# Kernel tuning notes

Measured on AMD Instinct MI355X. Metric: run time of the kernel, lower is better.

Reference implementation:

```python
import jax, jax.numpy as jnp
import numpy as np
import math

B, S, E, H = 4, 2048, 1024, 1024  # batch, seq, n_embd, head_size


def _rope(q, k, pos):
    # q, k: (B, S, H); pos: (B, S) float
    d = q.shape[-1]
    omega = 1.0 / (10000.0 ** (jnp.arange(d // 2, dtype=jnp.float32) / (d / 2.0)))
    ang = pos[..., None] * omega                      # (B, S, d/2)
    sin = jnp.sin(ang)
    cos = jnp.cos(ang)
    cos_pos = jnp.repeat(cos, 2, axis=-1)             # (B, S, d) [c0,c0,c1,c1,...]
    sin_pos = jnp.repeat(sin, 2, axis=-1)

    def rot(t):
        t_ = jnp.stack([-t[..., 1::2], t[..., 0::2]], axis=-1).reshape(t.shape)
        return t * cos_pos + t_ * sin_pos

    return rot(q), rot(k)


def setup_inputs() -> dict:
    key = jax.random.key(0)
    ks = jax.random.split(key, 9)
    s = 1.0 / math.sqrt(E)
    x = jax.random.normal(ks[0], (B, S, E), dtype=jnp.float32)
    pos = jnp.broadcast_to(jnp.arange(S, dtype=jnp.float32), (B, S))
    mask = jnp.triu(jnp.ones((S, S), dtype=bool), k=1)  # causal: True = masked out
    Wq = jax.random.normal(ks[1], (H, E), dtype=jnp.float32) * s
    Wk = jax.random.normal(ks[2], (H, E), dtype=jnp.float32) * s
    Wv = jax.random.normal(ks[3], (H, E), dtype=jnp.float32) * s
    bq = jax.random.normal(ks[4], (H,), dtype=jnp.float32) * 0.01
    bk = jax.random.normal(ks[5], (H,), dtype=jnp.float32) * 0.01
    bv = jax.random.normal(ks[6], (H,), dtype=jnp.float32) * 0.01
    Wo = jax.random.normal(ks[7], (H, H), dtype=jnp.float32) * (1.0 / math.sqrt(H))
    bo = jax.random.normal(ks[8], (H,), dtype=jnp.float32) * 0.01
    return {"x": x, "pos": pos, "mask": mask, "Wq": Wq, "bq": bq,
            "Wk": Wk, "bk": bk, "Wv": Wv, "bv": bv, "Wo": Wo, "bo": bo}


def reference(x, pos, mask, Wq, bq, Wk, bk, Wv, bv, Wo, bo):
    n_embd = x.shape[-1]
    q = jnp.einsum('bse,he->bsh', x, Wq) + bq
    k = jnp.einsum('bse,he->bsh', x, Wk) + bk
    v = jnp.einsum('bse,he->bsh', x, Wv) + bv
    q, k = _rope(q, k, pos)
    # NOTE: original divides by sqrt(x.shape[-1]) == sqrt(n_embd), not sqrt(head_size)
    w = jnp.einsum('bqh,bkh->bqk', q, k) / jnp.sqrt(jnp.float32(n_embd))
    w = jnp.where(mask, jnp.float32(-1e7), w)
    w = jax.nn.softmax(w, axis=-1)  # dropout is identity in eval mode
    out = jnp.einsum('bqk,bkh->bqh', w, v)
    out = jnp.einsum('bsh,oh->bso', out, Wo) + bo
    return out
```

## Files before the change

kernel.cpp:

```cpp
#include <hip/hip_runtime.h>
#include <hip/hip_bf16.h>
#include <stdint.h>

typedef __attribute__((ext_vector_type(4))) float  f32x4;
typedef __attribute__((ext_vector_type(8))) short  short8;
typedef __attribute__((ext_vector_type(8))) __bf16 bf16x8;

#define GLB_AS __attribute__((address_space(1)))
#define LDS_AS __attribute__((address_space(3)))

__device__ __forceinline__ float bf2f(ushort u) {
    union { uint u32; float f; } c; c.u32 = (uint)u << 16; return c.f;
}
__device__ __forceinline__ ushort f2bf(float f) {
    union { float f; uint u32; } c; c.f = f;
    uint x = c.u32;
    return (ushort)((x + 0x7fffu + ((x >> 16) & 1u)) >> 16);
}

__device__ __forceinline__ void storeC(float* p, float v)  { *p = v; }
__device__ __forceinline__ void storeC(ushort* p, float v) { *p = f2bf(v); }

template<int N> __device__ __forceinline__ void vmwait() {
    if constexpr (N == 0) asm volatile("s_waitcnt vmcnt(0)" ::: "memory");
    else if constexpr (N == 6) asm volatile("s_waitcnt vmcnt(6)" ::: "memory");
}

__global__ __launch_bounds__(256) void convert_f32_bf16(
    const float* __restrict__ in, ushort* __restrict__ out, long n)
{
    long i0 = ((long)blockIdx.x * 256 + threadIdx.x) * 8;
    long stride = (long)gridDim.x * 256 * 8;
    for (long i = i0; i < n; i += stride) {
        float4 a = *(const float4*)(in + i);
        float4 b = *(const float4*)(in + i + 4);
        short8 o;
        o[0] = (short)f2bf(a.x); o[1] = (short)f2bf(a.y);
        o[2] = (short)f2bf(a.z); o[3] = (short)f2bf(a.w);
        o[4] = (short)f2bf(b.x); o[5] = (short)f2bf(b.y);
        o[6] = (short)f2bf(b.z); o[7] = (short)f2bf(b.w);
        *(short8*)(out + i) = o;
    }
}

__global__ __launch_bounds__(256) void rope_inplace(
    ushort* __restrict__ qk, const float* __restrict__ pos)
{
    const int row = blockIdx.x;
    const float p = pos[row];
    const size_t base = (size_t)row * 2048;
    const int tid = threadIdx.x;
#pragma unroll
    for (int t = 0; t < 2; ++t) {
        int j = tid + t * 256;
        float omega = exp2f(-(float)j * (13.287712379549449f / 512.0f));
        float ang = p * omega;
        float sn, cs;
        sincosf(ang, &sn, &cs);
        uint pq = *(uint*)(qk + base + 2 * j);
        float q0 = bf2f((ushort)(pq & 0xffff)), q1 = bf2f((ushort)(pq >> 16));
        float r0 = q0 * cs - q1 * sn, r1 = q1 * cs + q0 * sn;
        *(uint*)(qk + base + 2 * j) = (uint)f2bf(r0) | ((uint)f2bf(r1) << 16);
        uint pk = *(uint*)(qk + base + 1024 + 2 * j);
        float k0 = bf2f((ushort)(pk & 0xffff)), k1 = bf2f((ushort)(pk >> 16));
        float s0 = k0 * cs - k1 * sn, s1 = k1 * cs + k0 * sn;
        *(uint*)(qk + base + 1024 + 2 * j) = (uint)f2bf(s0) | ((uint)f2bf(s1) << 16);
    }
}

__global__ __launch_bounds__(256) void softmax_rows(ushort* __restrict__ P)
{
    const size_t base = (size_t)blockIdx.x * 2048;
    const int tid = threadIdx.x;
    const int lane = tid & 63, wid = tid >> 6;
    short8 v = *(const short8*)(P + base + tid * 8);
    float f[8];
#pragma unroll
    for (int j = 0; j < 8; ++j) f[j] = bf2f((ushort)v[j]);
    float mx = f[0];
#pragma unroll
    for (int j = 1; j < 8; ++j) mx = fmaxf(mx, f[j]);
#pragma unroll
    for (int o = 32; o; o >>= 1) mx = fmaxf(mx, __shfl_xor(mx, o, 64));
    __shared__ float redm[4], reds[4];
    if (lane == 0) redm[wid] = mx;
    __syncthreads();
    mx = fmaxf(fmaxf(redm[0], redm[1]), fmaxf(redm[2], redm[3]));
    float s = 0.f;
#pragma unroll
    for (int j = 0; j < 8; ++j) { f[j] = __expf(f[j] - mx); s += f[j]; }
#pragma unroll
    for (int o = 32; o; o >>= 1) s += __shfl_xor(s, o, 64);
    if (lane == 0) reds[wid] = s;
    __syncthreads();
    s = reds[0] + reds[1] + reds[2] + reds[3];
    float inv = 1.0f / s;
    short8 o8;
#pragma unroll
    for (int j = 0; j < 8; ++j) o8[j] = (short)f2bf(f[j] * inv);
    *(short8*)(P + base + tid * 8) = o8;
}


template<int BUF, int HALF>
__device__ __forceinline__ void stageT(ushort (&L)[2][2][8192],
    const ushort* __restrict__ G, int tileBase, int ld, int tk,
    int wid, int sr, int scS)
{
#pragma unroll
    for (int i = 0; i < 2; ++i) {
        const int chunk = wid * 2 + i;
        const ushort* g = G + (size_t)(tileBase + HALF * 128 + chunk * 8 + sr) * ld
                        + tk * 64 + scS * 8;
        __builtin_amdgcn_global_load_lds((const GLB_AS void*)g,
            (LDS_AS void*)(&L[BUF][HALF][chunk * 512]), 16, 0, 0);
    }
}

template<int BUF, int HALF>
__device__ __forceinline__ void readA(const ushort (&As)[2][2][8192],
    short8 (&afr)[4][2], int wr, int fr, int kg)
{
    const int sw = (fr & 7) << 3;
#pragma unroll
    for (int m = 0; m < 4; ++m) {
        const int r = wr * 64 + m * 16 + fr;
#pragma unroll
        for (int kk = 0; kk < 2; ++kk)
            afr[m][kk] = *(const short8*)&As[BUF][HALF][r * 64 + ((kk * 32 + kg * 8) ^ sw)];
    }
}

template<int BUF, int HALF>
__device__ __forceinline__ void readB(const ushort (&Bs)[2][2][8192],
    short8 (&bfr)[2][2], int wc, int fr, int kg)
{
    const int sw = (fr & 7) << 3;
#pragma unroll
    for (int n = 0; n < 2; ++n) {
        const int r = wc * 32 + n * 16 + fr;
#pragma unroll
        for (int kk = 0; kk < 2; ++kk)
            bfr[n][kk] = *(const short8*)&Bs[BUF][HALF][r * 64 + ((kk * 32 + kg * 8) ^ sw)];
    }
}

template<int MQ, int NQ>
__device__ __forceinline__ void domfma(f32x4 (&acc)[2][2][4][2],
    const short8 (&afr)[4][2], const short8 (&bfr)[2][2])
{
#pragma unroll
    for (int kk = 0; kk < 2; ++kk)
#pragma unroll
        for (int m = 0; m < 4; ++m)
#pragma unroll
            for (int n = 0; n < 2; ++n)
                acc[MQ][NQ][m][n] = __builtin_amdgcn_mfma_f32_16x16x32_bf16(
                    __builtin_bit_cast(bf16x8, afr[m][kk]),
                    __builtin_bit_cast(bf16x8, bfr[n][kk]),
                    acc[MQ][NQ][m][n], 0, 0, 0);
}

#define PHASE_MID() \
    __builtin_amdgcn_s_barrier(); \
    asm volatile("s_waitcnt lgkmcnt(0)" ::: "memory"); \
    __builtin_amdgcn_sched_barrier(0); \
    __builtin_amdgcn_s_setprio(1)
#define PHASE_END() \
    __builtin_amdgcn_s_setprio(0); \
    __builtin_amdgcn_s_barrier()

template<int BUF, int MODE>
__device__ __forceinline__ void group(
    ushort (&As)[2][2][8192], ushort (&Bs)[2][2][8192],
    f32x4 (&acc)[2][2][4][2],
    const ushort* __restrict__ A, const ushort* __restrict__ B,
    int rowBase, int colBase, int lda, int ldb, int t,
    int wid, int wr, int wc, int fr, int kg, int sr, int scS)
{
    short8 afr[4][2], bfr[2][2];
    readA<BUF, 0>(As, afr, wr, fr, kg);
    readB<BUF, 0>(Bs, bfr, wc, fr, kg);
    if constexpr (MODE != 2) stageT<BUF ^ 1, 0>(As, A, rowBase, lda, t + 1, wid, sr, scS);
    asm volatile("s_waitcnt lgkmcnt(8)" ::: "memory");
    PHASE_MID();
    domfma<0, 0>(acc, afr, bfr);
    PHASE_END();
    readA<BUF, 1>(As, afr, wr, fr, kg);
    if constexpr (MODE == 0) stageT<BUF, 0>(Bs, B, colBase, ldb, t + 2, wid, sr, scS);
    PHASE_MID();
    domfma<1, 0>(acc, afr, bfr);
    PHASE_END();
    readB<BUF, 1>(Bs, bfr, wc, fr, kg);
    if constexpr (MODE == 0) stageT<BUF, 1>(As, A, rowBase, lda, t + 2, wid, sr, scS);
    PHASE_MID();
    domfma<1, 1>(acc, afr, bfr);
    PHASE_END();
    readA<BUF, 0>(As, afr, wr, fr, kg);
    if constexpr (MODE == 0) stageT<BUF, 1>(Bs, B, colBase, ldb, t + 2, wid, sr, scS);
    PHASE_MID();
    domfma<0, 1>(acc, afr, bfr);
    __builtin_amdgcn_s_setprio(0);
    if constexpr (MODE == 0) vmwait<6>();
    else if constexpr (MODE == 1) vmwait<0>();
    __builtin_amdgcn_s_barrier();
}

template<bool BIAS_COL, bool BIAS_ROW, bool CAUSAL_MASK, bool CAUSAL_K, typename OutT>
__global__ __launch_bounds__(512, 2) void gemm256(
    const ushort* __restrict__ A, const ushort* __restrict__ B,
    OutT* __restrict__ C, const float* __restrict__ bias,
    int K, int lda, int ldb, int ldc,
    long sA, long sB, long sC, float scale)
{
    __shared__ ushort As[2][2][8192];
    __shared__ ushort Bs[2][2][8192];

    const int nx = gridDim.x, ny = gridDim.y;
    int flat = blockIdx.x + nx * (blockIdx.y + ny * blockIdx.z);
    const int nwg = nx * ny * gridDim.z;
    const int qq = nwg >> 3;
    int swz = (flat & 7) * qq + (flat >> 3);
    const int bx = swz % nx;
    int rest = swz / nx;
    const int by = rest % ny;
    const int bz = rest / ny;

    A += (long)bz * sA;
    B += (long)bz * sB;
    C += (long)bz * sC;
    const int tid = threadIdx.x;
    const int lane = tid & 63;
    const int wid = tid >> 6;
    const int wr = wid >> 2, wc = wid & 3;
    const int rowBase = by * 256;
    const int colBase = bx * 256;
    const int fr = lane & 15;
    const int kg = lane >> 4;

    f32x4 acc[2][2][4][2] = {};

    const bool skip = CAUSAL_MASK && (colBase > rowBase + 255);
    int Kend = K;
    if (CAUSAL_K) { int ke = rowBase + 256; Kend = ke < K ? ke : K; }

    if (!skip) {
        const int sr = lane >> 3;
        const int scS = (lane & 7) ^ (lane >> 3);
        stageT<0, 0>(As, A, rowBase, lda, 0, wid, sr, scS);
        stageT<0, 0>(Bs, B, colBase, ldb, 0, wid, sr, scS);
        stageT<0, 1>(As, A, rowBase, lda, 0, wid, sr, scS);
        stageT<0, 1>(Bs, B, colBase, ldb, 0, wid, sr, scS);
        stageT<1, 0>(Bs, B, colBase, ldb, 1, wid, sr, scS);
        stageT<1, 1>(As, A, rowBase, lda, 1, wid, sr, scS);
        stageT<1, 1>(Bs, B, colBase, ldb, 1, wid, sr, scS);
        vmwait<6>();
        __builtin_amdgcn_s_barrier();

        const int NT = Kend >> 6;
        int t = 0;
        for (; t + 3 < NT; t += 2) {
            group<0, 0>(As, Bs, acc, A, B, rowBase, colBase, lda, ldb, t,
                        wid, wr, wc, fr, kg, sr, scS);
            group<1, 0>(As, Bs, acc, A, B, rowBase, colBase, lda, ldb, t + 1,
                        wid, wr, wc, fr, kg, sr, scS);
        }
        group<0, 1>(As, Bs, acc, A, B, rowBase, colBase, lda, ldb, t,
                    wid, wr, wc, fr, kg, sr, scS);
        group<1, 2>(As, Bs, acc, A, B, rowBase, colBase, lda, ldb, t + 1,
                    wid, wr, wc, fr, kg, sr, scS);
    }

#pragma unroll
    for (int mq = 0; mq < 2; ++mq)
#pragma unroll
        for (int nq = 0; nq < 2; ++nq)
#pragma unroll
            for (int m = 0; m < 4; ++m)
#pragma unroll
                for (int n = 0; n < 2; ++n)
#pragma unroll
                    for (int j = 0; j < 4; ++j) {
                        int row = rowBase + mq * 128 + wr * 64 + m * 16 + kg * 4 + j;
                        int col = colBase + nq * 128 + wc * 32 + n * 16 + fr;
                        float v = acc[mq][nq][m][n][j] * scale;
                        if (BIAS_COL) v += bias[col];
                        if (BIAS_ROW) v += bias[row];
                        if (CAUSAL_MASK && (col > row)) v = -1e7f;
                        storeC(C + (size_t)row * ldc + col, v);
                    }
}

extern "C" void kernel_launch(void* const* d_in, const int* in_sizes, int n_in,
                              void* d_out, int out_size, void* d_ws, size_t ws_size,
                              hipStream_t stream)
{
    const float* x   = (const float*)d_in[0];
    const float* pos = (const float*)d_in[1];
    const float* Wq = (const float*)d_in[3]; const float* bq = (const float*)d_in[4];
    const float* Wk = (const float*)d_in[5]; const float* bk = (const float*)d_in[6];
    const float* Wv = (const float*)d_in[7]; const float* bv = (const float*)d_in[8];
    const float* Wo = (const float*)d_in[9]; const float* bo = (const float*)d_in[10];
    float* out = (float*)d_out;

    const int S = 2048, E = 1024, H = 1024, Bz = 4;
    const int Mtot = Bz * S;

    ushort* xb   = (ushort*)d_ws;
    ushort* wqkb = xb   + (size_t)Mtot * E;
    ushort* wvb  = wqkb + (size_t)2 * H * E;
    ushort* wob  = wvb  + (size_t)H * E;
    ushort* qk   = wob  + (size_t)H * H;
    ushort* vt   = qk   + (size_t)Mtot * 2 * H;
    ushort* P    = vt   + (size_t)H * Mtot;
    float*  bqk  = (float*)(P + (size_t)Bz * S * S);
    ushort* O    = xb;

    convert_f32_bf16<<<2048, 256, 0, stream>>>(x,  xb,   (long)Mtot * E);
    convert_f32_bf16<<<512,  256, 0, stream>>>(Wq, wqkb, (long)H * E);
    convert_f32_bf16<<<512,  256, 0, stream>>>(Wk, wqkb + (size_t)H * E, (long)H * E);
    convert_f32_bf16<<<512,  256, 0, stream>>>(Wv, wvb,  (long)H * E);
    convert_f32_bf16<<<512,  256, 0, stream>>>(Wo, wob,  (long)H * H);
    hipMemcpyAsync(bqk,     bq, H * sizeof(float), hipMemcpyDeviceToDevice, stream);
    hipMemcpyAsync(bqk + H, bk, H * sizeof(float), hipMemcpyDeviceToDevice, stream);

    gemm256<true, false, false, false, ushort><<<dim3(8, 32, 1), 512, 0, stream>>>(
        xb, wqkb, qk, bqk, E, E, E, 2 * H, 0, 0, 0, 1.0f);
    gemm256<false, true, false, false, ushort><<<dim3(32, 4, 1), 512, 0, stream>>>(
        wvb, xb, vt, bv, E, E, E, Mtot, 0, 0, 0, 1.0f);

    rope_inplace<<<Mtot, 256, 0, stream>>>(qk, pos);

    gemm256<false, false, true, false, ushort><<<dim3(8, 8, Bz), 512, 0, stream>>>(
        qk, qk + H, P, nullptr, H, 2 * H, 2 * H, S,
        (long)S * 2 * H, (long)S * 2 * H, (long)S * S, 0.03125f);

    softmax_rows<<<Mtot, 256, 0, stream>>>(P);

    gemm256<false, false, false, true, ushort><<<dim3(4, 8, Bz), 512, 0, stream>>>(
        P, vt, O, nullptr, S, S, Mtot, H,
        (long)S * S, (long)S, (long)S * H, 1.0f);

    gemm256<true, false, false, false, float><<<dim3(4, 32, 1), 512, 0, stream>>>(
        O, wob, out, bo, H, H, H, H, 0, 0, 0, 1.0f);
}
```

Before: 382.5 us.

## Add simple 128x128 GEMM kernel for V, PV and output projections

Adds a simpler 128x128-tile GEMM with 256 threads and single-buffered LDS staging, and uses it for the V projection, the P·V product and the output projection to get more workgroups and better load balance on small grids. The 256-tile kernel drops its row-bias and causal-K paths, its launch bounds go from 2 to 1 waves per SIMD, its A fragments are double-buffered to save one LDS reread per group, and a sched_barrier is removed. The new kernel has no prefetch overlap and uses unswizzled LDS layouts that may cause bank conflicts.

Measured after the change: 342.2 us. -10.5%, faster.

```diff
diff --git a/kernel.cpp b/kernel.cpp
--- a/kernel.cpp
+++ b/kernel.cpp
@@ -101,6 +101,90 @@
     *(short8*)(P + base + tid * 8) = o8;
 }
 
+template<bool BIAS_COL, bool BIAS_ROW, bool CAUSAL_MASK, bool CAUSAL_K, typename OutT>
+__global__ __launch_bounds__(256, 2) void gemm_bt(
+    const ushort* __restrict__ A, const ushort* __restrict__ B,
+    OutT* __restrict__ C, const float* __restrict__ bias,
+    int K, int lda, int ldb, int ldc,
+    long sA, long sB, long sC, float scale)
+{
+    __shared__ ushort As[128 * 64];
+    __shared__ ushort Bs[128 * 64];
+    A += (long)blockIdx.z * sA;
+    B += (long)blockIdx.z * sB;
+    C += (long)blockIdx.z * sC;
+    const int tid = threadIdx.x;
+    const int lane = tid & 63;
+    const int wid = tid >> 6;
+    const int rowBase = blockIdx.y * 128;
+    const int colBase = blockIdx.x * 128;
+    const int wr = (wid >> 1) * 64;
+    const int wc = (wid & 1) * 64;
+    const int fr = lane & 15;
+    const int kg = lane >> 4;
+
+    f32x4 acc[4][4] = {};
+
+    bool skip = false;
+    if (CAUSAL_MASK) skip = (colBase > rowBase + 127);
+    int Kend = K;
+    if (CAUSAL_K) { int ke = rowBase + 128; Kend = ke < K ? ke : K; }
+
+    if (!skip) {
+        const int sRow = lane >> 3;
+        const int sCol = (lane & 7) * 8;
+        for (int k0 = 0; k0 < Kend; k0 += 64) {
+            __syncthreads();
+#pragma unroll
+            for (int r = 0; r < 4; ++r) {
+                const int chunk = wid * 4 + r;
+                const ushort* ga = A + (size_t)(rowBase + chunk * 8 + sRow) * lda + k0 + sCol;
+                __builtin_amdgcn_global_load_lds((const GLB_AS void*)ga,
+                    (LDS_AS void*)(As + chunk * 512), 16, 0, 0);
+                const ushort* gb = B + (size_t)(colBase + chunk * 8 + sRow) * ldb + k0 + sCol;
+                __builtin_amdgcn_global_load_lds((const GLB_AS void*)gb,
+                    (LDS_AS void*)(Bs + chunk * 512), 16, 0, 0);
+            }
+            __syncthreads();
+#pragma unroll
+            for (int kk = 0; kk < 64; kk += 32) {
+                short8 a[4], b[4];
+#pragma unroll
+                for (int m = 0; m < 4; ++m)
+                    a[m] = *(const short8*)&As[(wr + m * 16 + fr) * 64 + kk + kg * 8];
+#pragma unroll
+                for (int n = 0; n < 4; ++n)
+                    b[n] = *(const short8*)&Bs[(wc + n * 16 + fr) * 64 + kk + kg * 8];
+#pragma unroll
+                for (int m = 0; m < 4; ++m)
+#pragma unroll
+                    for (int n = 0; n < 4; ++n)
+                        acc[m][n] = __builtin_amdgcn_mfma_f32_16x16x32_bf16(
+                            __builtin_bit_cast(bf16x8, a[m]),
+                            __builtin_bit_cast(bf16x8, b[n]),
+                            acc[m][n], 0, 0, 0);
+            }
+        }
+    }
+
+#pragma unroll
+    for (int m = 0; m < 4; ++m) {
+#pragma unroll
+        for (int n = 0; n < 4; ++n) {
+#pragma unroll
+            for (int j = 0; j < 4; ++j) {
+                int row = rowBase + wr + m * 16 + kg * 4 + j;
+                int col = colBase + wc + n * 16 + fr;
+                float v = acc[m][n][j] * scale;
+                if (BIAS_COL) v += bias[col];
+                if (BIAS_ROW) v += bias[row];
+                if (CAUSAL_MASK && (col > row)) v = -1e7f;
+                storeC(C + (size_t)row * ldc + col, v);
+            }
+        }
+    }
+}
+
 
 template<int BUF, int HALF>
 __device__ __forceinline__ void stageT(ushort (&L)[2][2][8192],
@@ -164,7 +248,6 @@
 #define PHASE_MID() \
     __builtin_amdgcn_s_barrier(); \
     asm volatile("s_waitcnt lgkmcnt(0)" ::: "memory"); \
-    __builtin_amdgcn_sched_barrier(0); \
     __builtin_amdgcn_s_setprio(1)
 #define PHASE_END() \
     __builtin_amdgcn_s_setprio(0); \
@@ -178,36 +261,35 @@
     int rowBase, int colBase, int lda, int ldb, int t,
     int wid, int wr, int wc, int fr, int kg, int sr, int scS)
 {
-    short8 afr[4][2], bfr[2][2];
-    readA<BUF, 0>(As, afr, wr, fr, kg);
+    short8 afrA[4][2], afrB[4][2], bfr[2][2];
+    readA<BUF, 0>(As, afrA, wr, fr, kg);
     readB<BUF, 0>(Bs, bfr, wc, fr, kg);
     if constexpr (MODE != 2) stageT<BUF ^ 1, 0>(As, A, rowBase, lda, t + 1, wid, sr, scS);
     asm volatile("s_waitcnt lgkmcnt(8)" ::: "memory");
     PHASE_MID();
-    domfma<0, 0>(acc, afr, bfr);
+    domfma<0, 0>(acc, afrA, bfr);
     PHASE_END();
-    readA<BUF, 1>(As, afr, wr, fr, kg);
+    readA<BUF, 1>(As, afrB, wr, fr, kg);
     if constexpr (MODE == 0) stageT<BUF, 0>(Bs, B, colBase, ldb, t + 2, wid, sr, scS);
     PHASE_MID();
-    domfma<1, 0>(acc, afr, bfr);
+    domfma<1, 0>(acc, afrB, bfr);
     PHASE_END();
     readB<BUF, 1>(Bs, bfr, wc, fr, kg);
     if constexpr (MODE == 0) stageT<BUF, 1>(As, A, rowBase, lda, t + 2, wid, sr, scS);
     PHASE_MID();
-    domfma<1, 1>(acc, afr, bfr);
+    domfma<1, 1>(acc, afrB, bfr);
     PHASE_END();
-    readA<BUF, 0>(As, afr, wr, fr, kg);
     if constexpr (MODE == 0) stageT<BUF, 1>(Bs, B, colBase, ldb, t + 2, wid, sr, scS);
     PHASE_MID();
-    domfma<0, 1>(acc, afr, bfr);
+    domfma<0, 1>(acc, afrA, bfr);
     __builtin_amdgcn_s_setprio(0);
     if constexpr (MODE == 0) vmwait<6>();
     else if constexpr (MODE == 1) vmwait<0>();
     __builtin_amdgcn_s_barrier();
 }
 
-template<bool BIAS_COL, bool BIAS_ROW, bool CAUSAL_MASK, bool CAUSAL_K, typename OutT>
-__global__ __launch_bounds__(512, 2) void gemm256(
+template<bool BIAS_COL, bool CAUSAL_MASK, typename OutT>
+__global__ __launch_bounds__(512, 1) void gemm256(
     const ushort* __restrict__ A, const ushort* __restrict__ B,
     OutT* __restrict__ C, const float* __restrict__ bias,
     int K, int lda, int ldb, int ldc,
@@ -241,8 +323,6 @@
     f32x4 acc[2][2][4][2] = {};
 
     const bool skip = CAUSAL_MASK && (colBase > rowBase + 255);
-    int Kend = K;
-    if (CAUSAL_K) { int ke = rowBase + 256; Kend = ke < K ? ke : K; }
 
     if (!skip) {
         const int sr = lane >> 3;
@@ -257,7 +337,7 @@
         vmwait<6>();
         __builtin_amdgcn_s_barrier();
 
-        const int NT = Kend >> 6;
+        const int NT = K >> 6;
         int t = 0;
         for (; t + 3 < NT; t += 2) {
             group<0, 0>(As, Bs, acc, A, B, rowBase, colBase, lda, ldb, t,
@@ -285,7 +365,6 @@
                         int col = colBase + nq * 128 + wc * 32 + n * 16 + fr;
                         float v = acc[mq][nq][m][n][j] * scale;
                         if (BIAS_COL) v += bias[col];
-                        if (BIAS_ROW) v += bias[row];
                         if (CAUSAL_MASK && (col > row)) v = -1e7f;
                         storeC(C + (size_t)row * ldc + col, v);
                     }
@@ -324,23 +403,23 @@
     hipMemcpyAsync(bqk,     bq, H * sizeof(float), hipMemcpyDeviceToDevice, stream);
     hipMemcpyAsync(bqk + H, bk, H * sizeof(float), hipMemcpyDeviceToDevice, stream);
 
-    gemm256<true, false, false, false, ushort><<<dim3(8, 32, 1), 512, 0, stream>>>(
+    gemm256<true, false, ushort><<<dim3(8, 32, 1), 512, 0, stream>>>(
         xb, wqkb, qk, bqk, E, E, E, 2 * H, 0, 0, 0, 1.0f);
-    gemm256<false, true, false, false, ushort><<<dim3(32, 4, 1), 512, 0, stream>>>(
+    gemm_bt<false, true, false, false, ushort><<<dim3(64, 8, 1), 256, 0, stream>>>(
         wvb, xb, vt, bv, E, E, E, Mtot, 0, 0, 0, 1.0f);
 
     rope_inplace<<<Mtot, 256, 0, stream>>>(qk, pos);
 
-    gemm256<false, false, true, false, ushort><<<dim3(8, 8, Bz), 512, 0, stream>>>(
+    gemm256<false, true, ushort><<<dim3(8, 8, Bz), 512, 0, stream>>>(
         qk, qk + H, P, nullptr, H, 2 * H, 2 * H, S,
         (long)S * 2 * H, (long)S * 2 * H, (long)S * S, 0.03125f);
 
     softmax_rows<<<Mtot, 256, 0, stream>>>(P);
 
-    gemm256<false, false, false, true, ushort><<<dim3(4, 8, Bz), 512, 0, stream>>>(
+    gemm_bt<false, false, false, true, ushort><<<dim3(8, 16, Bz), 256, 0, stream>>>(
         P, vt, O, nullptr, S, S, Mtot, H,
         (long)S * S, (long)S, (long)S * H, 1.0f);
 
-    gemm256<true, false, false, false, float><<<dim3(4, 32, 1), 512, 0, stream>>>(
+    gemm_bt<true, false, false, false, float><<<dim3(8, 64, 1), 256, 0, stream>>>(
         O, wob, out, bo, H, H, H, H, 0, 0, 0, 1.0f);
 }
```
